# Kernel optimization log

Measured on AMD Instinct MI355X. Metric: run time of the kernel, lower is better.

## Reference

```python
import jax, jax.numpy as jnp
import numpy as np

PAD = 0
C_CONST = 0.1712209


def setup_inputs() -> dict:
    key = jax.random.key(0)
    ks = jax.random.split(key, 6)
    tlen, bsz, slen, hsize, vocab = 64, 32, 64, 1024, 32000
    hidden = jax.random.normal(ks[0], (tlen, bsz, hsize), dtype=jnp.float32)
    context = jax.random.normal(ks[1], (slen, bsz, hsize), dtype=jnp.float32)
    src = jax.random.randint(ks[2], (bsz, slen), 0, vocab, dtype=jnp.int64)
    stdv = 1.0 / np.sqrt(hsize)
    W_gen = jax.random.uniform(ks[3], (vocab, hsize), dtype=jnp.float32, minval=-stdv, maxval=stdv)
    b_gen = jnp.zeros((vocab,), dtype=jnp.float32)
    # Xavier-like init for the copy gate
    w_copy = jax.random.normal(ks[4], (hsize,), dtype=jnp.float32) * np.sqrt(2.0 / (hsize + 1))
    b_copy = jnp.zeros((1,), dtype=jnp.float32)
    return {"hidden": hidden, "context": context, "src": src,
            "W_gen": W_gen, "b_gen": b_gen, "w_copy": w_copy, "b_copy": b_copy}


def reference(hidden, context, src, W_gen, b_gen, w_copy, b_copy):
    tlen, bsz, hsize = hidden.shape
    # p(z=1): probability of copying, [tlen, bsz, 1]
    copy_prob = jax.nn.sigmoid(jnp.einsum('tbh,h->tb', hidden, w_copy) + b_copy[0])[..., None]
    # generator distribution over tgt vocab
    logits = jnp.einsum('tbh,vh->tbv', hidden, W_gen) + b_gen
    prob = jax.nn.softmax(logits.astype(jnp.float32), axis=-1)
    p_g = prob * (1.0 - copy_prob)  # [tlen, bsz, vocab]
    # copy attention over source positions: bmm(query[b,t,h], keys[b,s,h]^T)
    attn_score = jnp.einsum('tbh,sbh->bts', hidden, context)  # [bsz, tlen, slen]
    src_mask = (src == PAD)[:, None, :]  # [bsz, 1, slen]
    attn_score = jnp.where(src_mask, -jnp.inf, attn_score.astype(jnp.float32))
    attns = jax.nn.softmax(attn_score, axis=-1)  # [bsz, tlen, slen]
    p_c = jnp.transpose(attns, (1, 0, 2)) * copy_prob  # [tlen, bsz, slen]
    # scatter_add copy probs into vocab distribution along dim 2
    slen = src.shape[1]
    idx_src = jnp.broadcast_to(src[None, :, :], (tlen, bsz, slen))
    t_idx = jnp.arange(tlen)[:, None, None]
    b_idx = jnp.arange(bsz)[None, :, None]
    p_g = p_g.at[t_idx, b_idx, idx_src].add(p_c)
    return jnp.log(p_g) + C_CONST
```

## Files before the change

kernel.cpp:

```cpp
#include <hip/hip_runtime.h>
#include <hip/hip_bf16.h>
#include <stdint.h>

#define TLEN 64
#define BSZ 32
#define SLEN 64
#define HS 1024
#define VOC 32000
#define NROW (TLEN*BSZ)
#define C_CONST_F 0.1712209f

#define BM 256
#define BN 256
#define BKT 32
#define NKT (HS/BKT)
#define SLOT_BYTES 32768
#define B_REGION 16384

typedef __attribute__((ext_vector_type(8))) short short8;
typedef __attribute__((ext_vector_type(4))) float f32x4;

static __device__ __forceinline__ ushort f2bf(float f) {
    uint32_t u = __builtin_bit_cast(uint32_t, f);
    uint32_t r = (u + 0x7fffu + ((u >> 16) & 1u)) >> 16;
    return (ushort)r;
}
static __device__ __forceinline__ float bf2f(ushort u) {
    uint32_t v = ((uint32_t)u) << 16;
    return __builtin_bit_cast(float, v);
}
static __device__ __forceinline__ void async16(const void* g, void* lds) {
    __builtin_amdgcn_global_load_lds(
        (const __attribute__((address_space(1))) void*)g,
        (__attribute__((address_space(3))) void*)lds, 16, 0, 0);
}
static __device__ __forceinline__ int swz12(int e) { return e ^ (((e >> 4) & 15) << 1); }

#define ATTN_BLOCKS 128
#define A_PAIRS 262144

__global__ __launch_bounds__(256) void pre_kernel(const float* __restrict__ hidden,
                                                  const float* __restrict__ context,
                                                  const int* __restrict__ src,
                                                  const float* __restrict__ w_copy,
                                                  const float* __restrict__ b_copy,
                                                  const float* __restrict__ W_gen,
                                                  float* __restrict__ cp,
                                                  float* __restrict__ p_c,
                                                  ushort* __restrict__ dst) {
    __shared__ float hb[3][16][36];
    __shared__ float cb[3][64][36];
    __shared__ float wb[3][32];
    __shared__ float sc[16][65];
    __shared__ float gred[16];
    __shared__ float cps[16];
    __shared__ int   sbuf[SLEN];

    int tid = threadIdx.x;
    if (blockIdx.x >= ATTN_BLOCKS) {
        int p = (blockIdx.x - ATTN_BLOCKS) * 256 + tid;
        const float* sp = (p < A_PAIRS) ? (hidden + (size_t)p * 8)
                                        : (W_gen + (size_t)(p - A_PAIRS) * 8);
        float4 v0 = *(const float4*)sp;
        float4 v1 = *(const float4*)(sp + 4);
        short8 o;
        o[0] = (short)f2bf(v0.x); o[1] = (short)f2bf(v0.y);
        o[2] = (short)f2bf(v0.z); o[3] = (short)f2bf(v0.w);
        o[4] = (short)f2bf(v1.x); o[5] = (short)f2bf(v1.y);
        o[6] = (short)f2bf(v1.z); o[7] = (short)f2bf(v1.w);
        *(short8*)(dst + (size_t)p * 8) = o;
        return;
    }

    int b  = blockIdx.x >> 2;
    int tq = blockIdx.x & 3;
    int wid = tid >> 6, lane = tid & 63;
    int lr = lane & 15, lg = lane >> 4;

    if (tid < SLEN) sbuf[tid] = src[b * SLEN + tid];

    const int cidx0 = tid * 2;
    const int cs0 = cidx0 >> 3, ck0 = cidx0 & 7;
    const int cs1 = (cidx0 + 1) >> 3, ck1 = (cidx0 + 1) & 7;
    const float* cbase = context + (size_t)b * HS;
    const float* hbase = hidden + ((size_t)(tq * 16) * 32 + b) * HS;

    float4 rc0, rc1, rh, rw;
#define ALOAD(I)                                                                   \
    {                                                                              \
        rc0 = *(const float4*)(cbase + (size_t)cs0 * 32 * HS + (I) * 32 + ck0 * 4);\
        rc1 = *(const float4*)(cbase + (size_t)cs1 * 32 * HS + (I) * 32 + ck1 * 4);\
        if (tid < 128) rh = *(const float4*)(hbase + (size_t)(tid >> 3) * 32 * HS + (I) * 32 + (tid & 7) * 4); \
        if (tid < 8)  rw = *(const float4*)(w_copy + (I) * 32 + tid * 4);          \
    }
#define AWRITE(BUF)                                                                \
    {                                                                              \
        *(float4*)(&cb[BUF][cs0][ck0 * 4]) = rc0;                                  \
        *(float4*)(&cb[BUF][cs1][ck1 * 4]) = rc1;                                  \
        if (tid < 128) *(float4*)(&hb[BUF][tid >> 3][(tid & 7) * 4]) = rh;         \
        if (tid < 8)  *(float4*)(&wb[BUF][tid * 4]) = rw;                          \
    }

    f32x4 acc = f32x4{0.f, 0.f, 0.f, 0.f};
    float greg = 0.f;
    int gt = lane >> 2, gk = lane & 3;

    ALOAD(0); AWRITE(0);
    ALOAD(1); AWRITE(1);
    ALOAD(2);
    __syncthreads();

    for (int i = 0; i < 32; ++i) {
        int buf = i % 3;
        float4 a0 = *(const float4*)(&hb[buf][lr][lg * 8]);
        float4 a1 = *(const float4*)(&hb[buf][lr][lg * 8 + 4]);
        float4 b0 = *(const float4*)(&cb[buf][wid * 16 + lr][lg * 8]);
        float4 b1 = *(const float4*)(&cb[buf][wid * 16 + lr][lg * 8 + 4]);
        short8 ahi, alo, bhi, blo;
        float af[8] = {a0.x, a0.y, a0.z, a0.w, a1.x, a1.y, a1.z, a1.w};
        float bf[8] = {b0.x, b0.y, b0.z, b0.w, b1.x, b1.y, b1.z, b1.w};
        #pragma unroll
        for (int e = 0; e < 8; ++e) {
            uint32_t ua = __builtin_bit_cast(uint32_t, af[e]);
            ahi[e] = (short)(ua >> 16);
            alo[e] = (short)f2bf(af[e] - __builtin_bit_cast(float, ua & 0xffff0000u));
            uint32_t ub = __builtin_bit_cast(uint32_t, bf[e]);
            bhi[e] = (short)(ub >> 16);
            blo[e] = (short)f2bf(bf[e] - __builtin_bit_cast(float, ub & 0xffff0000u));
        }
        acc = __builtin_amdgcn_mfma_f32_16x16x32_bf16(ahi, bhi, acc, 0, 0, 0);
        acc = __builtin_amdgcn_mfma_f32_16x16x32_bf16(ahi, blo, acc, 0, 0, 0);
        acc = __builtin_amdgcn_mfma_f32_16x16x32_bf16(alo, bhi, acc, 0, 0, 0);
        if (wid == 0) {
            #pragma unroll
            for (int e = 0; e < 8; ++e)
                greg += hb[buf][gt][gk * 8 + e] * wb[buf][gk * 8 + e];
        }
        if (i + 2 < 32) {
            AWRITE((i + 2) % 3);
            if (i + 3 < 32) ALOAD(i + 3);
        }
        __syncthreads();
    }
#undef ALOAD
#undef AWRITE

    if (wid == 0) {
        greg += __shfl_xor(greg, 1, 64);
        greg += __shfl_xor(greg, 2, 64);
        if (gk == 0) gred[gt] = greg;
    }
    #pragma unroll
    for (int r = 0; r < 4; ++r)
        sc[lg * 4 + r][wid * 16 + lr] = acc[r];
    __syncthreads();
    if (tid < 16) {
        float s = 1.f / (1.f + expf(-(gred[tid] + b_copy[0])));
        cps[tid] = s;
        cp[(size_t)(tq * 16 + tid) * 32 + b] = s;
    }
    __syncthreads();
    {
        int t = tid >> 4, e = tid & 15;
        float v[4];
        float mx = -INFINITY;
        #pragma unroll
        for (int i = 0; i < 4; ++i) {
            v[i] = sc[t][e * 4 + i];
            if (sbuf[e * 4 + i] == 0) v[i] = -INFINITY;
            mx = fmaxf(mx, v[i]);
        }
        for (int k = 8; k >= 1; k >>= 1) mx = fmaxf(mx, __shfl_xor(mx, k, 16));
        float se = 0.f;
        #pragma unroll
        for (int i = 0; i < 4; ++i) { v[i] = __expf(v[i] - mx); se += v[i]; }
        for (int k = 8; k >= 1; k >>= 1) se += __shfl_xor(se, k, 16);
        float g = cps[t] / se;
        int row = (tq * 16 + t) * 32 + b;
        float4 o; o.x = v[0] * g; o.y = v[1] * g; o.z = v[2] * g; o.w = v[3] * g;
        *(float4*)(p_c + (size_t)row * SLEN + e * 4) = o;
    }
}

template <bool BF16L>
__global__ __launch_bounds__(512, 2) void gemm_kernel(const ushort* __restrict__ A,
                                                      const ushort* __restrict__ B,
                                                      const float* __restrict__ b_gen,
                                                      void* __restrict__ logits,
                                                      float* __restrict__ partials ) {
    __shared__ ushort sAB[4 * SLOT_BYTES / 2];

    int orig = blockIdx.x;
    int wg = (orig & 7) * 125 + (orig >> 3);
    int mIdx = wg & 7;
    int nIdx = wg >> 3;
    int m0 = mIdx * BM, n0 = nIdx * BN;
    int tid = threadIdx.x, wid = tid >> 6, lane = tid & 63;
    int wm = (wid >> 2) * 128, wn = (wid & 3) * 64;
    int lr = lane & 15, lg = lane >> 4;

    const ushort* gA[2]; const ushort* gB[2];
    uint32_t ldsOffA[2], ldsOffB[2];
    #pragma unroll
    for (int j = 0; j < 2; ++j) {
        int s = j * 512 + tid;
        int row = s >> 2;
        int kc = (s & 3) ^ ((row >> 1) & 3);
        gA[j] = A + (size_t)(m0 + row) * HS + kc * 8;
        gB[j] = B + (size_t)(n0 + row) * HS + kc * 8;
        ldsOffA[j] = (uint32_t)((j * 512 + wid * 64) * 16);
        ldsOffB[j] = (uint32_t)(B_REGION + (j * 512 + wid * 64) * 16);
    }

    uint32_t kcs   = (uint32_t)((lg ^ ((lr >> 1) & 3)) * 16);
    uint32_t offAb = (uint32_t)(wm + lr) * 64 + kcs;
    uint32_t offBb = B_REGION + (uint32_t)(wn + lr) * 64 + kcs;

    f32x4 acc[8][4];
    #pragma unroll
    for (int m = 0; m < 8; ++m)
        #pragma unroll
        for (int n = 0; n < 4; ++n) acc[m][n] = f32x4{0.f, 0.f, 0.f, 0.f};

#define STAGE(KT)                                                          \
    {                                                                      \
        char* sd = (char*)sAB + ((KT) & 3) * SLOT_BYTES;                   \
        int k0s = (KT) * BKT;                                              \
        _Pragma("unroll")                                                  \
        for (int j = 0; j < 2; ++j) {                                      \
            async16(gA[j] + k0s, sd + ldsOffA[j]);                         \
            async16(gB[j] + k0s, sd + ldsOffB[j]);                         \
        }                                                                  \
    }

#define PHASE_BODY(KT, DOSTAGE)                                                        \
    {                                                                                  \
        const char* sl = (const char*)sAB + ((KT) & 3) * SLOT_BYTES;                   \
        short8 af[8], bv[4];                                                           \
        _Pragma("unroll")                                                              \
        for (int mb = 0; mb < 8; ++mb)                                                 \
            af[mb] = *(const short8*)(sl + offAb + mb * 1024);                         \
        _Pragma("unroll")                                                              \
        for (int nb = 0; nb < 4; ++nb)                                                 \
            bv[nb] = *(const short8*)(sl + offBb + nb * 1024);                         \
        if (DOSTAGE) STAGE((KT) + 3);                                                  \
        _Pragma("unroll")                                                              \
        for (int mb = 0; mb < 8; ++mb)                                                 \
            _Pragma("unroll")                                                          \
            for (int nb = 0; nb < 4; ++nb)                                             \
                acc[mb][nb] = __builtin_amdgcn_mfma_f32_16x16x32_bf16(af[mb], bv[nb],  \
                                                                     acc[mb][nb], 0, 0, 0); \
    }

#define GATE8 asm volatile("s_waitcnt vmcnt(8)\n\ts_barrier" ::: "memory")

    STAGE(0); STAGE(1); STAGE(2);

    for (int kb = 0; kb < 7; ++kb) {
        int kt = kb * 4;
        GATE8; PHASE_BODY(kt + 0, true);
        GATE8; PHASE_BODY(kt + 1, true);
        GATE8; PHASE_BODY(kt + 2, true);
        GATE8; PHASE_BODY(kt + 3, true);
    }
    GATE8; PHASE_BODY(28, true);
    GATE8; PHASE_BODY(29, false);
    asm volatile("s_waitcnt vmcnt(4)\n\ts_barrier" ::: "memory");
    PHASE_BODY(30, false);
    asm volatile("s_waitcnt vmcnt(0)\n\ts_barrier" ::: "memory");
    PHASE_BODY(31, false);
#undef PHASE_BODY
#undef STAGE
#undef GATE8

    asm volatile("s_barrier" ::: "memory");

    float bg[4];
    #pragma unroll
    for (int nb = 0; nb < 4; ++nb) bg[nb] = b_gen[n0 + wn + nb * 16 + lr];
    int chunk = nIdx * 4 + (wid & 3);
    ushort* stile = sAB + wid * 8192;

    #pragma unroll
    for (int mb = 0; mb < 8; ++mb) {
        #pragma unroll
        for (int r = 0; r < 4; ++r) {
            int rl = mb * 16 + lg * 4 + r;
            int row = m0 + wm + rl;
            float v[4];
            float mx = -INFINITY;
            #pragma unroll
            for (int nb = 0; nb < 4; ++nb) {
                v[nb] = acc[mb][nb][r] + bg[nb];
                mx = fmaxf(mx, v[nb]);
            }
            if (BF16L) {
                #pragma unroll
                for (int nb = 0; nb < 4; ++nb) {
                    int cl = nb * 16 + lr;
                    int slot_w = (cl >> 3) ^ (rl & 7);
                    stile[rl * 64 + slot_w * 8 + (cl & 7)] = f2bf(v[nb]);
                }
            } else {
                float* outp = (float*)logits;
                #pragma unroll
                for (int nb = 0; nb < 4; ++nb)
                    outp[(size_t)row * VOC + n0 + wn + nb * 16 + lr] = v[nb];
            }
            for (int k = 8; k >= 1; k >>= 1) mx = fmaxf(mx, __shfl_xor(mx, k, 16));
            float se = 0.f;
            #pragma unroll
            for (int nb = 0; nb < 4; ++nb) se += __expf(v[nb] - mx);
            for (int k = 8; k >= 1; k >>= 1) se += __shfl_xor(se, k, 16);
            if (lr == 0) {
                float2 pv; pv.x = mx; pv.y = se;
                *(float2*)(partials + ((size_t)row * 500 + chunk) * 2) = pv;
            }
        }
    }
    if (BF16L) {
        ushort* Lbf = (ushort*)logits;
        #pragma unroll
        for (int rep = 0; rep < 16; ++rep) {
            int idx = rep * 64 + lane;
            int rl = idx >> 3, c8 = idx & 7;
            int slot_r = c8 ^ (rl & 7);
            short8 val = *(const short8*)(stile + rl * 64 + slot_r * 8);
            ushort* dst = Lbf + (size_t)(m0 + wm + rl) * VOC + n0 + wn + c8 * 8;
            *(short8*)dst = val;
        }
    }
}

__global__ __launch_bounds__(256) void reduce_kernel(const float* __restrict__ partials,
                                                     float* __restrict__ Ms,
                                                     float* __restrict__ Ss) {
    int wid = threadIdx.x >> 6, lane = threadIdx.x & 63;
    int row = blockIdx.x * 4 + wid;
    float m = -INFINITY, s = 0.f;
    for (int c = lane; c < 500; c += 64) {
        float2 p = *(const float2*)(partials + ((size_t)row * 500 + c) * 2);
        float nm = fmaxf(m, p.x);
        s = s * __expf(m - nm) + p.y * __expf(p.x - nm);
        m = nm;
    }
    for (int k = 32; k >= 1; k >>= 1) {
        float om = __shfl_xor(m, k, 64), os = __shfl_xor(s, k, 64);
        float nm = fmaxf(m, om);
        s = s * __expf(m - nm) + os * __expf(om - nm);
        m = nm;
    }
    if (lane == 0) { Ms[row] = m; Ss[row] = s; }
}

template <bool BF16L>
__global__ __launch_bounds__(256) void finalize_kernel(const int* __restrict__ src,
                                                       const float* __restrict__ p_c,
                                                       const float* __restrict__ cp,
                                                       const float* __restrict__ Ms,
                                                       const float* __restrict__ Ss,
                                                       const void* __restrict__ logits,
                                                       float* __restrict__ out) {
    int row = blockIdx.y;
    int c0 = blockIdx.x * 4096;
    int b = row & (BSZ - 1);
    __shared__ float addv[4096];
    int tid = threadIdx.x;
    for (int i = tid; i < 4096; i += 256) addv[i] = 0.f;
    __syncthreads();
    if (tid < SLEN) {
        int v = src[b * SLEN + tid];
        if (v >= c0 && v < c0 + 4096)
            atomicAdd(&addv[swz12(v - c0)], p_c[row * SLEN + tid]);
    }
    __syncthreads();
    int col = c0 + tid * 16;
    if (col >= VOC) return;
    float M = Ms[row];
    float g = (1.f - cp[row]) / Ss[row];
    float L[16];
    if (BF16L) {
        const ushort* lb = (const ushort*)logits + (size_t)row * VOC + col;
        short8 a = *(const short8*)lb;
        short8 c = *(const short8*)(lb + 8);
        for (int i = 0; i < 8; ++i) { L[i] = bf2f((ushort)a[i]); L[8 + i] = bf2f((ushort)c[i]); }
    } else {
        const float* lf = (const float*)logits + (size_t)row * VOC + col;
        for (int i = 0; i < 4; ++i) {
            float4 v = *(const float4*)(lf + i * 4);
            L[i * 4 + 0] = v.x; L[i * 4 + 1] = v.y; L[i * 4 + 2] = v.z; L[i * 4 + 3] = v.w;
        }
    }
    float res[16];
    for (int i = 0; i < 16; ++i) {
        float p = __expf(L[i] - M) * g + addv[swz12(tid * 16 + i)];
        res[i] = __logf(p) + C_CONST_F;
    }
    float* op = out + (size_t)row * VOC + col;
    for (int i = 0; i < 4; ++i) {
        float4 v;
        v.x = res[i * 4 + 0]; v.y = res[i * 4 + 1]; v.z = res[i * 4 + 2]; v.w = res[i * 4 + 3];
        *(float4*)(op + i * 4) = v;
    }
}

extern "C" void kernel_launch(void* const* d_in, const int* in_sizes, int n_in,
                              void* d_out, int out_size, void* d_ws, size_t ws_size,
                              hipStream_t stream) {
    const float* hidden  = (const float*)d_in[0];
    const float* context = (const float*)d_in[1];
    const int*   src     = (const int*)d_in[2];
    const float* W_gen   = (const float*)d_in[3];
    const float* b_gen   = (const float*)d_in[4];
    const float* w_copy  = (const float*)d_in[5];
    const float* b_copy  = (const float*)d_in[6];
    float* out = (float*)d_out;
    char* ws = (char*)d_ws;

    float*  cp       = (float*)(ws);
    float*  p_c      = (float*)(ws + 8192);
    float*  Ms       = (float*)(ws + 532480);
    float*  Ss       = (float*)(ws + 540672);
    float*  partials = (float*)(ws + 548864);
    ushort* Abf      = (ushort*)(ws + 8740864);
    const size_t NEED_BF16 = 209543168;
    ushort* Lbf      = (ushort*)(ws + 78471168);

    int preGrid = ATTN_BLOCKS + (NROW * HS + VOC * HS) / 8 / 256;
    pre_kernel<<<preGrid, 256, 0, stream>>>(hidden, context, src, w_copy, b_copy,
                                            W_gen, cp, p_c, Abf);

    int ggrid = (NROW / BM) * (VOC / BN);
    dim3 fgrid(8, NROW);
    const ushort* Wb = (const ushort*)(ws + 12935168);
    if (ws_size >= NEED_BF16) {
        gemm_kernel<true><<<ggrid, 512, 0, stream>>>(Abf, Wb, b_gen, Lbf, partials);
        reduce_kernel<<<NROW / 4, 256, 0, stream>>>(partials, Ms, Ss);
        finalize_kernel<true><<<fgrid, 256, 0, stream>>>(src, p_c, cp, Ms, Ss, Lbf, out);
    } else {
        gemm_kernel<false><<<ggrid, 512, 0, stream>>>(Abf, Wb, b_gen, out, partials);
        reduce_kernel<<<NROW / 4, 256, 0, stream>>>(partials, Ms, Ss);
        finalize_kernel<false><<<fgrid, 256, 0, stream>>>(src, p_c, cp, Ms, Ss, out, out);
    }
}
```

Before: 316.5 us.

## Halve GEMM LDS to a double buffer and raise occupancy target to four blocks

The GEMM shrinks its shared-memory ring from four 32 KB stages to two, prefetching one k-tile ahead and waiting on all outstanding loads before each step instead of keeping three tiles in flight. The bf16 logits epilogue is split into two passes of 64 rows so its staging tile fits the smaller LDS. The launch bound is raised to four 512-thread blocks per CU to trade pipeline depth for occupancy. With a 128-float accumulator per thread, the lower register budget this bound implies risks spilling, and the full vmcnt(0) wait exposes global-load latency.

```diff
diff --git a/kernel.cpp b/kernel.cpp
--- a/kernel.cpp
+++ b/kernel.cpp
@@ -183,12 +183,12 @@
 }
 
 template <bool BF16L>
-__global__ __launch_bounds__(512, 2) void gemm_kernel(const ushort* __restrict__ A,
+__global__ __launch_bounds__(512, 4) void gemm_kernel(const ushort* __restrict__ A,
                                                       const ushort* __restrict__ B,
                                                       const float* __restrict__ b_gen,
                                                       void* __restrict__ logits,
                                                       float* __restrict__ partials ) {
-    __shared__ ushort sAB[4 * SLOT_BYTES / 2];
+    __shared__ ushort sAB[2 * SLOT_BYTES / 2];
 
     int orig = blockIdx.x;
     int wg = (orig & 7) * 125 + (orig >> 3);
@@ -224,7 +224,7 @@
 
 #define STAGE(KT)                                                          \
     {                                                                      \
-        char* sd = (char*)sAB + ((KT) & 3) * SLOT_BYTES;                   \
+        char* sd = (char*)sAB + ((KT) & 1) * SLOT_BYTES;                   \
         int k0s = (KT) * BKT;                                              \
         _Pragma("unroll")                                                  \
         for (int j = 0; j < 2; ++j) {                                      \
@@ -235,7 +235,7 @@
 
 #define PHASE_BODY(KT, DOSTAGE)                                                        \
     {                                                                                  \
-        const char* sl = (const char*)sAB + ((KT) & 3) * SLOT_BYTES;                   \
+        const char* sl = (const char*)sAB + ((KT) & 1) * SLOT_BYTES;                   \
         short8 af[8], bv[4];                                                           \
         _Pragma("unroll")                                                              \
         for (int mb = 0; mb < 8; ++mb)                                                 \
@@ -243,7 +243,7 @@
         _Pragma("unroll")                                                              \
         for (int nb = 0; nb < 4; ++nb)                                                 \
             bv[nb] = *(const short8*)(sl + offBb + nb * 1024);                         \
-        if (DOSTAGE) STAGE((KT) + 3);                                                  \
+        if (DOSTAGE) STAGE((KT) + 1);                                                  \
         _Pragma("unroll")                                                              \
         for (int mb = 0; mb < 8; ++mb)                                                 \
             _Pragma("unroll")                                                          \
@@ -252,26 +252,18 @@
                                                                      acc[mb][nb], 0, 0, 0); \
     }
 
-#define GATE8 asm volatile("s_waitcnt vmcnt(8)\n\ts_barrier" ::: "memory")
-
-    STAGE(0); STAGE(1); STAGE(2);
-
-    for (int kb = 0; kb < 7; ++kb) {
-        int kt = kb * 4;
-        GATE8; PHASE_BODY(kt + 0, true);
-        GATE8; PHASE_BODY(kt + 1, true);
-        GATE8; PHASE_BODY(kt + 2, true);
-        GATE8; PHASE_BODY(kt + 3, true);
-    }
-    GATE8; PHASE_BODY(28, true);
-    GATE8; PHASE_BODY(29, false);
-    asm volatile("s_waitcnt vmcnt(4)\n\ts_barrier" ::: "memory");
-    PHASE_BODY(30, false);
-    asm volatile("s_waitcnt vmcnt(0)\n\ts_barrier" ::: "memory");
-    PHASE_BODY(31, false);
+#define GATE0 asm volatile("s_waitcnt vmcnt(0)\n\ts_barrier" ::: "memory")
+
+    STAGE(0);
+
+    for (int kb = 0; kb < 16; ++kb) {
+        int kt = kb * 2;
+        GATE0; PHASE_BODY(kt + 0, true);
+        GATE0; PHASE_BODY(kt + 1, kb < 15);
+    }
 #undef PHASE_BODY
 #undef STAGE
-#undef GATE8
+#undef GATE0
 
     asm volatile("s_barrier" ::: "memory");
 
@@ -279,55 +271,59 @@
     #pragma unroll
     for (int nb = 0; nb < 4; ++nb) bg[nb] = b_gen[n0 + wn + nb * 16 + lr];
     int chunk = nIdx * 4 + (wid & 3);
-    ushort* stile = sAB + wid * 8192;
+    ushort* stile = sAB + wid * 4096;
 
     #pragma unroll
-    for (int mb = 0; mb < 8; ++mb) {
+    for (int pass = 0; pass < 2; ++pass) {
         #pragma unroll
-        for (int r = 0; r < 4; ++r) {
-            int rl = mb * 16 + lg * 4 + r;
-            int row = m0 + wm + rl;
-            float v[4];
-            float mx = -INFINITY;
+        for (int mbl = 0; mbl < 4; ++mbl) {
+            int mb = pass * 4 + mbl;
             #pragma unroll
-            for (int nb = 0; nb < 4; ++nb) {
-                v[nb] = acc[mb][nb][r] + bg[nb];
-                mx = fmaxf(mx, v[nb]);
-            }
-            if (BF16L) {
+            for (int r = 0; r < 4; ++r) {
+                int rl = mbl * 16 + lg * 4 + r;
+                int row = m0 + wm + pass * 64 + rl;
+                float v[4];
+                float mx = -INFINITY;
                 #pragma unroll
                 for (int nb = 0; nb < 4; ++nb) {
-                    int cl = nb * 16 + lr;
-                    int slot_w = (cl >> 3) ^ (rl & 7);
-                    stile[rl * 64 + slot_w * 8 + (cl & 7)] = f2bf(v[nb]);
+                    v[nb] = acc[mb][nb][r] + bg[nb];
+                    mx = fmaxf(mx, v[nb]);
                 }
-            } else {
-                float* outp = (float*)logits;
+                if (BF16L) {
+                    #pragma unroll
+                    for (int nb = 0; nb < 4; ++nb) {
+                        int cl = nb * 16 + lr;
+                        int slot_w = (cl >> 3) ^ (rl & 7);
+                        stile[rl * 64 + slot_w * 8 + (cl & 7)] = f2bf(v[nb]);
+                    }
+                } else {
+                    float* outp = (float*)logits;
+                    #pragma unroll
+                    for (int nb = 0; nb < 4; ++nb)
+                        outp[(size_t)row * VOC + n0 + wn + nb * 16 + lr] = v[nb];
+                }
+                for (int k = 8; k >= 1; k >>= 1) mx = fmaxf(mx, __shfl_xor(mx, k, 16));
+                float se = 0.f;
                 #pragma unroll
-                for (int nb = 0; nb < 4; ++nb)
-                    outp[(size_t)row * VOC + n0 + wn + nb * 16 + lr] = v[nb];
+                for (int nb = 0; nb < 4; ++nb) se += __expf(v[nb] - mx);
+                for (int k = 8; k >= 1; k >>= 1) se += __shfl_xor(se, k, 16);
+                if (lr == 0) {
+                    float2 pv; pv.x = mx; pv.y = se;
+                    *(float2*)(partials + ((size_t)row * 500 + chunk) * 2) = pv;
+                }
             }
-            for (int k = 8; k >= 1; k >>= 1) mx = fmaxf(mx, __shfl_xor(mx, k, 16));
-            float se = 0.f;
+        }
+        if (BF16L) {
+            ushort* Lbf = (ushort*)logits;
             #pragma unroll
-            for (int nb = 0; nb < 4; ++nb) se += __expf(v[nb] - mx);
-            for (int k = 8; k >= 1; k >>= 1) se += __shfl_xor(se, k, 16);
-            if (lr == 0) {
-                float2 pv; pv.x = mx; pv.y = se;
-                *(float2*)(partials + ((size_t)row * 500 + chunk) * 2) = pv;
+            for (int rep = 0; rep < 8; ++rep) {
+                int idx = rep * 64 + lane;
+                int rl = idx >> 3, c8 = idx & 7;
+                int slot_r = c8 ^ (rl & 7);
+                short8 val = *(const short8*)(stile + rl * 64 + slot_r * 8);
+                ushort* dst = Lbf + (size_t)(m0 + wm + pass * 64 + rl) * VOC + n0 + wn + c8 * 8;
+                *(short8*)dst = val;
             }
-        }
-    }
-    if (BF16L) {
-        ushort* Lbf = (ushort*)logits;
-        #pragma unroll
-        for (int rep = 0; rep < 16; ++rep) {
-            int idx = rep * 64 + lane;
-            int rl = idx >> 3, c8 = idx & 7;
-            int slot_r = c8 ^ (rl & 7);
-            short8 val = *(const short8*)(stile + rl * 64 + slot_r * 8);
-            ushort* dst = Lbf + (size_t)(m0 + wm + rl) * VOC + n0 + wn + c8 * 8;
-            *(short8*)dst = val;
         }
     }
 }
```

Result: slower. 1.235 ms (+290.3%).
